# Optimization experiments

Measured on AMD Instinct MI355X. Metric: run time of the kernel, lower is better.

## Reference

```python
import jax, jax.numpy as jnp
import numpy as np
from jax import lax

N_STATE = 1024
N_HEAD = 16
H_DIM = N_STATE // N_HEAD  # 64
NUM_ROT = 8
BASE = 10000.0
B, S = 4, 4096


def setup_inputs() -> dict:
    key = jax.random.key(0)
    k1, k2, k3 = jax.random.split(key, 3)
    x = jax.random.normal(k1, (B, S, N_STATE), dtype=jnp.float32)
    thetas = jax.random.normal(k2, (NUM_ROT,), dtype=jnp.float32) * 0.1
    # torch: torch.rand(num_rotations, 2) * h_dim -> floats in [0, h_dim)
    rotation_pairs = jax.random.uniform(k3, (NUM_ROT, 2), dtype=jnp.float32) * H_DIM
    theta_scale = jnp.ones((1,), dtype=jnp.float32)
    rotation_matrix = jnp.eye(H_DIM, dtype=jnp.float32)
    inv_freq = 1.0 / BASE ** (jnp.arange(0, H_DIM, 2, dtype=jnp.float32) / H_DIM)
    return {"x": x, "thetas": thetas, "rotation_pairs": rotation_pairs,
            "theta_scale": theta_scale, "rotation_matrix": rotation_matrix,
            "inv_freq": inv_freq}


def _compose_rotation(thetas, idx, theta_scale, rotation_matrix, dtype):
    """Compose all Givens rotations + final learned rotation into one [h,h] matrix.
    Matmul is associative, so R = G_0 @ G_1 @ ... @ G_{K-1} @ rotation_matrix,
    then x @ R equals the original sequential (x @ G_k) loop."""
    eye = jnp.eye(H_DIM, dtype=dtype)

    def step(R, inp):
        i, j, theta = inp
        c, s = jnp.cos(theta), jnp.sin(theta)
        # sequential .at sets replicate torch's in-place assignment order
        G = eye.at[i, i].set(c).at[i, j].set(-s).at[j, i].set(s).at[j, j].set(c)
        return R @ G, None

    R, _ = lax.scan(step, eye, (idx[:, 0], idx[:, 1], thetas * theta_scale[0]))
    return R @ rotation_matrix


def reference(x, thetas, rotation_pairs, theta_scale, rotation_matrix, inv_freq):
    b, s, n_state = x.shape
    idx = rotation_pairs.astype(jnp.int32)  # torch .long() truncation of positive floats
    R = _compose_rotation(thetas, idx, theta_scale, rotation_matrix, x.dtype)
    xh = x.reshape(b, s, N_HEAD, H_DIM) @ R  # [b,s,h,d] @ [d,d]
    # rotary sin/cos
    pos = jnp.arange(s, dtype=inv_freq.dtype)
    sinusoid = pos[:, None] * inv_freq[None, :]          # [s, d/2]
    sin = jnp.sin(sinusoid)[None, :, None, :]
    cos = jnp.cos(sinusoid)[None, :, None, :]
    x1, x2 = xh[..., ::2], xh[..., 1::2]
    out = jnp.concatenate([x1 * cos - x2 * sin, x1 * sin + x2 * cos], axis=-1)
    return out.reshape(b, s, n_state)
```

## Files before the change

### kernel.cpp

```cpp
#include <hip/hip_runtime.h>
#include <hip/hip_bf16.h>
#include <math.h>

#define N_STATE 1024
#define N_HEAD  16
#define H_DIM   64
#define NUM_ROT 8
#define SEQ     4096
#define HVPB    128
#define TILES   2

typedef __attribute__((ext_vector_type(8))) short bf16x8;
typedef __attribute__((ext_vector_type(4))) float f32x4;

__device__ __forceinline__ unsigned short f2bf(float f) {
    union { float f; unsigned u; } v; v.f = f;
    unsigned r = v.u + 0x7fffu + ((v.u >> 16) & 1u);
    return (unsigned short)(r >> 16);
}
__device__ __forceinline__ unsigned cvtpk(float a, float b) {
    union { __hip_bfloat162 h; unsigned u; } p;
    p.h = __float22bfloat162_rn(make_float2(a, b));
    return p.u;
}
__device__ __forceinline__ bf16x8 cvt8(const float4 lo, const float4 hi) {
    union { bf16x8 v; unsigned u[4]; } r;
    r.u[0] = cvtpk(lo.x, lo.y);
    r.u[1] = cvtpk(lo.z, lo.w);
    r.u[2] = cvtpk(hi.x, hi.y);
    r.u[3] = cvtpk(hi.z, hi.w);
    return r.v;
}

#define RF_STRIDE 68
#define RT_STRIDE 72
#define SM_TOTAL 26752

__global__ __launch_bounds__(256, 4)
void rope_fused_kernel(const float* __restrict__ x,
                       const float* __restrict__ thetas,
                       const float* __restrict__ pairs,
                       const float* __restrict__ theta_scale,
                       const float* __restrict__ M,
                       const float* __restrict__ inv_freq,
                       float* __restrict__ out,
                       int nb)
{
    __shared__ __align__(16) char smem[SM_TOTAL];
    float*          Rf   = (float*)(smem);
    unsigned short* Rt_s = (unsigned short*)(smem + 17408);
    float*          csh  = (float*)(smem + 26624);
    int*            prs  = (int*)(smem + 26688);
    float*          snc  = (float*)(smem);

    const int t   = threadIdx.x;
    const int w   = t >> 6;
    const int l   = t & 63;
    const int r16 = l & 15;
    const int q4  = l >> 4;
    const int bid = blockIdx.x;

    float4 xa[4], xb[4];
    {
        const size_t rA = (size_t)bid * HVPB + w * 32;
        const float* pA = x + (rA + r16) * H_DIM + q4 * 8;
        xa[0] = *(const float4*)(pA);
        xa[1] = *(const float4*)(pA + 4);
        xa[2] = *(const float4*)(pA + 32);
        xa[3] = *(const float4*)(pA + 36);
        const size_t rB = rA + 16;
        const float* pB = x + (rB + r16) * H_DIM + q4 * 8;
        xb[0] = *(const float4*)(pB);
        xb[1] = *(const float4*)(pB + 4);
        xb[2] = *(const float4*)(pB + 32);
        xb[3] = *(const float4*)(pB + 36);
    }

    float am[2][8];
    #pragma unroll
    for (int kh = 0; kh < 2; ++kh)
        #pragma unroll
        for (int e = 0; e < 8; ++e)
            am[kh][e] = M[(kh * 32 + q4 * 8 + e) * H_DIM + w * 16 + r16];

    if (t < NUM_ROT) {
        float sv, cv;
        sincosf(thetas[t] * theta_scale[0], &sv, &cv);
        csh[2 * t] = cv; csh[2 * t + 1] = sv;
    }
    if (t < 2 * NUM_ROT) prs[t] = (int)pairs[t];
    #pragma unroll
    for (int q = 0; q < 17; ++q) Rf[t + q * 256] = 0.0f;
    __syncthreads();

    if (t < H_DIM) {
        float* myrow = &Rf[t * RF_STRIDE];
        myrow[t] = 1.0f;
        #pragma unroll
        for (int k = 0; k < NUM_ROT; ++k) {
            const int   i = prs[2 * k], j = prs[2 * k + 1];
            const float c = csh[2 * k], s = csh[2 * k + 1];
            const float ri = myrow[i], rj = myrow[j];
            if (i == j) {
                myrow[i] = c * ri;
            } else {
                myrow[i] =  c * ri + s * rj;
                myrow[j] = -s * ri + c * rj;
            }
        }
    }
    __syncthreads();

    {
        bf16x8 ca[2];
        #pragma unroll
        for (int kh = 0; kh < 2; ++kh)
            ca[kh] = cvt8(make_float4(am[kh][0], am[kh][1], am[kh][2], am[kh][3]),
                          make_float4(am[kh][4], am[kh][5], am[kh][6], am[kh][7]));
        f32x4 dacc[4];
        #pragma unroll
        for (int j = 0; j < 4; ++j) {
            f32x4 z = {0.f, 0.f, 0.f, 0.f};
            #pragma unroll
            for (int kh = 0; kh < 2; ++kh) {
                const float* rp = &Rf[(j * 16 + r16) * RF_STRIDE + kh * 32 + q4 * 8];
                const float4 f0 = *(const float4*)(rp);
                const float4 f1 = *(const float4*)(rp + 4);
                z = __builtin_amdgcn_mfma_f32_16x16x32_bf16(ca[kh], cvt8(f0, f1),
                                                            z, 0, 0, 0);
            }
            dacc[j] = z;
        }
        #pragma unroll
        for (int j = 0; j < 4; ++j) {
            #pragma unroll
            for (int r = 0; r < 4; ++r) {
                const int f = w * 16 + q4 * 4 + r;
                const int p = ((f & 1) << 5) | (f >> 1);
                Rt_s[p * RT_STRIDE + j * 16 + r16] = f2bf(dacc[j][r]);
            }
        }
    }

    const int srl = t >> 5;
    const int sf  = t & 31;
    float svv[TILES], cvv[TILES];
    {
        const float fr = inv_freq[sf];
        #pragma unroll
        for (int tt = 0; tt < TILES; ++tt) {
            const int pos = ((bid + tt * nb) * 8 + srl) & (SEQ - 1);
            sincosf((float)pos * fr, &svv[tt], &cvv[tt]);
        }
    }
    __syncthreads();

    #pragma unroll
    for (int tt = 0; tt < TILES; ++tt) {
        snc[tt * 512 + srl * 64 + sf]      = svv[tt];
        snc[tt * 512 + srl * 64 + 32 + sf] = cvv[tt];
    }
    bf16x8 afr[4][2];
    #pragma unroll
    for (int mt = 0; mt < 4; ++mt)
        #pragma unroll
        for (int kh = 0; kh < 2; ++kh)
            afr[mt][kh] = *(const bf16x8*)(
                &Rt_s[(mt * 16 + r16) * RT_STRIDE + kh * 32 + q4 * 8]);
    __syncthreads();

    #pragma unroll
    for (int c = 0; c < 2 * TILES; ++c) {
        const int tt = c >> 1, nt = c & 1;
        const size_t row0 = (size_t)(bid + tt * nb) * HVPB + w * 32 + nt * 16;

        float4 xn[4];
        if (c + 2 < 2 * TILES) {
            const int c2 = c + 2;
            const int tt2 = c2 >> 1, nt2 = c2 & 1;
            const size_t r2 = (size_t)(bid + tt2 * nb) * HVPB + w * 32 + nt2 * 16;
            const float* rp = x + (r2 + r16) * H_DIM + q4 * 8;
            xn[0] = *(const float4*)(rp);
            xn[1] = *(const float4*)(rp + 4);
            xn[2] = *(const float4*)(rp + 32);
            xn[3] = *(const float4*)(rp + 36);
        }

        const bf16x8 b0 = cvt8(xa[0], xa[1]);
        const bf16x8 b1 = cvt8(xa[2], xa[3]);

        f32x4 acc[4];
        #pragma unroll
        for (int mt = 0; mt < 4; ++mt) {
            f32x4 z = {0.0f, 0.0f, 0.0f, 0.0f};
            z = __builtin_amdgcn_mfma_f32_16x16x32_bf16(afr[mt][0], b0, z, 0, 0, 0);
            z = __builtin_amdgcn_mfma_f32_16x16x32_bf16(afr[mt][1], b1, z, 0, 0, 0);
            acc[mt] = z;
        }

        const int pl = tt * 512 + (w * 2 + nt) * 64;
        float* op = out + (row0 + r16) * H_DIM;
        #pragma unroll
        for (int half = 0; half < 2; ++half) {
            const int p0 = half * 16 + q4 * 4;
            const float4 sn = *(const float4*)(&snc[pl + p0]);
            const float4 cs = *(const float4*)(&snc[pl + 32 + p0]);
            const f32x4 a1 = acc[half];
            const f32x4 a2 = acc[half + 2];
            float4 olo, ohi;
            olo.x = a1.x * cs.x - a2.x * sn.x;
            olo.y = a1.y * cs.y - a2.y * sn.y;
            olo.z = a1.z * cs.z - a2.z * sn.z;
            olo.w = a1.w * cs.w - a2.w * sn.w;
            ohi.x = a1.x * sn.x + a2.x * cs.x;
            ohi.y = a1.y * sn.y + a2.y * cs.y;
            ohi.z = a1.z * sn.z + a2.z * cs.z;
            ohi.w = a1.w * sn.w + a2.w * cs.w;
            *(float4*)(op + p0)      = olo;
            *(float4*)(op + 32 + p0) = ohi;
        }

        #pragma unroll
        for (int i = 0; i < 4; ++i) { xa[i] = xb[i]; }
        if (c + 2 < 2 * TILES) {
            #pragma unroll
            for (int i = 0; i < 4; ++i) xb[i] = xn[i];
        }
    }
}

extern "C" void kernel_launch(void* const* d_in, const int* in_sizes, int n_in,
                              void* d_out, int out_size, void* d_ws, size_t ws_size,
                              hipStream_t stream)
{
    const float* x      = (const float*)d_in[0];
    const float* thetas = (const float*)d_in[1];
    const float* pairs  = (const float*)d_in[2];
    const float* tscale = (const float*)d_in[3];
    const float* M      = (const float*)d_in[4];
    const float* invf   = (const float*)d_in[5];
    float* out = (float*)d_out;

    const int n_hv   = in_sizes[0] / H_DIM;
    const int blocks = n_hv / (HVPB * TILES);
    rope_fused_kernel<<<blocks, 256, 0, stream>>>(x, thetas, pairs, tscale,
                                                  M, invf, out, blocks);
}
```

Before: 26.62 us.

## Process one tile per block, doubling grid size and raising occupancy hint

Each block now handles a single 128-head-vector tile instead of two, so the grid doubles and the in-loop prefetch of the next tile's x goes away. Launch bounds move from 4 to 5 blocks per SM to allow more resident blocks. In exchange, the per-block setup (composing the rotation matrix, its MFMA product with M, and the sin/cos table) is repeated twice as often across the grid, and there is less overlap of global loads within a block.

```diff
diff --git a/kernel.cpp b/kernel.cpp
--- a/kernel.cpp
+++ b/kernel.cpp
@@ -8,7 +8,6 @@
 #define NUM_ROT 8
 #define SEQ     4096
 #define HVPB    128
-#define TILES   2
 
 typedef __attribute__((ext_vector_type(8))) short bf16x8;
 typedef __attribute__((ext_vector_type(4))) float f32x4;
@@ -36,15 +35,14 @@
 #define RT_STRIDE 72
 #define SM_TOTAL 26752
 
-__global__ __launch_bounds__(256, 4)
+__global__ __launch_bounds__(256, 5)
 void rope_fused_kernel(const float* __restrict__ x,
                        const float* __restrict__ thetas,
                        const float* __restrict__ pairs,
                        const float* __restrict__ theta_scale,
                        const float* __restrict__ M,
                        const float* __restrict__ inv_freq,
-                       float* __restrict__ out,
-                       int nb)
+                       float* __restrict__ out)
 {
     __shared__ __align__(16) char smem[SM_TOTAL];
     float*          Rf   = (float*)(smem);
@@ -68,8 +66,7 @@
         xa[1] = *(const float4*)(pA + 4);
         xa[2] = *(const float4*)(pA + 32);
         xa[3] = *(const float4*)(pA + 36);
-        const size_t rB = rA + 16;
-        const float* pB = x + (rB + r16) * H_DIM + q4 * 8;
+        const float* pB = pA + 16 * H_DIM;
         xb[0] = *(const float4*)(pB);
         xb[1] = *(const float4*)(pB + 4);
         xb[2] = *(const float4*)(pB + 32);
@@ -144,22 +141,15 @@
 
     const int srl = t >> 5;
     const int sf  = t & 31;
-    float svv[TILES], cvv[TILES];
+    float sv_, cv_;
     {
-        const float fr = inv_freq[sf];
-        #pragma unroll
-        for (int tt = 0; tt < TILES; ++tt) {
-            const int pos = ((bid + tt * nb) * 8 + srl) & (SEQ - 1);
-            sincosf((float)pos * fr, &svv[tt], &cvv[tt]);
-        }
-    }
-    __syncthreads();
-
-    #pragma unroll
-    for (int tt = 0; tt < TILES; ++tt) {
-        snc[tt * 512 + srl * 64 + sf]      = svv[tt];
-        snc[tt * 512 + srl * 64 + 32 + sf] = cvv[tt];
-    }
+        const int pos = (bid * 8 + srl) & (SEQ - 1);
+        sincosf((float)pos * inv_freq[sf], &sv_, &cv_);
+    }
+    __syncthreads();
+
+    snc[srl * 64 + sf]      = sv_;
+    snc[srl * 64 + 32 + sf] = cv_;
     bf16x8 afr[4][2];
     #pragma unroll
     for (int mt = 0; mt < 4; ++mt)
@@ -170,24 +160,12 @@
     __syncthreads();
 
     #pragma unroll
-    for (int c = 0; c < 2 * TILES; ++c) {
-        const int tt = c >> 1, nt = c & 1;
-        const size_t row0 = (size_t)(bid + tt * nb) * HVPB + w * 32 + nt * 16;
-
-        float4 xn[4];
-        if (c + 2 < 2 * TILES) {
-            const int c2 = c + 2;
-            const int tt2 = c2 >> 1, nt2 = c2 & 1;
-            const size_t r2 = (size_t)(bid + tt2 * nb) * HVPB + w * 32 + nt2 * 16;
-            const float* rp = x + (r2 + r16) * H_DIM + q4 * 8;
-            xn[0] = *(const float4*)(rp);
-            xn[1] = *(const float4*)(rp + 4);
-            xn[2] = *(const float4*)(rp + 32);
-            xn[3] = *(const float4*)(rp + 36);
-        }
-
-        const bf16x8 b0 = cvt8(xa[0], xa[1]);
-        const bf16x8 b1 = cvt8(xa[2], xa[3]);
+    for (int nt = 0; nt < 2; ++nt) {
+        const size_t row0 = (size_t)bid * HVPB + w * 32 + nt * 16;
+        const float4* xd = (nt == 0) ? xa : xb;
+
+        const bf16x8 b0 = cvt8(xd[0], xd[1]);
+        const bf16x8 b1 = cvt8(xd[2], xd[3]);
 
         f32x4 acc[4];
         #pragma unroll
@@ -198,7 +176,7 @@
             acc[mt] = z;
         }
 
-        const int pl = tt * 512 + (w * 2 + nt) * 64;
+        const int pl = (w * 2 + nt) * 64;
         float* op = out + (row0 + r16) * H_DIM;
         #pragma unroll
         for (int half = 0; half < 2; ++half) {
@@ -219,13 +197,6 @@
             *(float4*)(op + p0)      = olo;
             *(float4*)(op + 32 + p0) = ohi;
         }
-
-        #pragma unroll
-        for (int i = 0; i < 4; ++i) { xa[i] = xb[i]; }
-        if (c + 2 < 2 * TILES) {
-            #pragma unroll
-            for (int i = 0; i < 4; ++i) xb[i] = xn[i];
-        }
     }
 }
 
@@ -242,7 +213,7 @@
     float* out = (float*)d_out;
 
     const int n_hv   = in_sizes[0] / H_DIM;
-    const int blocks = n_hv / (HVPB * TILES);
+    const int blocks = n_hv / HVPB;
     rope_fused_kernel<<<blocks, 256, 0, stream>>>(x, thetas, pairs, tscale,
-                                                  M, invf, out, blocks);
-}
+                                                  M, invf, out);
+}
```

After: 28.81 us. 1.08x slower.
